# Kernel tuning notes

Measured on AMD Instinct MI355X. Metric: run time of the kernel, lower is better.

## Reference

```python
import jax, jax.numpy as jnp
import numpy as np

B, T, D, F, C = 32768, 256, 10, 512, 1  # batch, trees, max_depth, features, classes
LVL_PAD = T * 2 ** (D - 1)  # padded width of per-level node/bias tables


def setup_inputs() -> dict:
    key = jax.random.key(0)
    k = jax.random.split(key, 6)
    x = jax.random.normal(k[0], (B, F), dtype=jnp.float32)
    root_nodes = jax.random.randint(k[1], (T,), 0, F, dtype=jnp.int32)
    root_biases = jax.random.normal(k[2], (T,), dtype=jnp.float32)
    # levels 1..D-1 packed into a padded matrix; level i uses first T*2**i entries
    nodes = jax.random.randint(k[3], (D - 1, LVL_PAD), 0, F, dtype=jnp.int32)
    biases = jax.random.normal(k[4], (D - 1, LVL_PAD), dtype=jnp.float32)
    leaf_nodes = jax.random.normal(k[5], (T * 2 ** D, C), dtype=jnp.float32)
    return {"x": x, "root_nodes": root_nodes, "root_biases": root_biases,
            "nodes": nodes, "biases": biases, "leaf_nodes": leaf_nodes}


def reference(x, root_nodes, root_biases, nodes, biases, leaf_nodes):
    b = x.shape[0]
    t = root_nodes.shape[0]
    depth = nodes.shape[0] + 1
    tree_indices = 2 * jnp.arange(t, dtype=jnp.int32)  # [T]
    # root level: cond(x[:, root_nodes], root_biases) -> child index offset per tree
    prev = (x[:, root_nodes] <= root_biases).astype(jnp.int32) + tree_indices  # [B, T]
    prev = prev.reshape(-1)  # [B*T]
    for i in range(1, depth):
        width = t * (2 ** i)
        lvl_nodes = nodes[i - 1, :width]    # [T*2^i]
        lvl_biases = biases[i - 1, :width]  # [T*2^i]
        gather_idx = lvl_nodes[prev].reshape(b, t)              # [B, T] feature ids
        feats = jnp.take_along_axis(x, gather_idx, axis=1).reshape(-1)  # [B*T]
        cond = (feats <= lvl_biases[prev]).astype(jnp.int32)
        prev = 2 * prev + cond
    out = leaf_nodes[prev].reshape(b, t, -1)  # [B, T, C]
    return out
```

## Files before the change

kernel.cpp:

```cpp
#include <hip/hip_runtime.h>

constexpr int kB = 32768;
constexpr int kT = 256;
constexpr int kD = 10;
constexpr int kF = 512;
constexpr int kLvlPad = kT << (kD - 1);
constexpr int kLevels = kD - 1;

constexpr int kRows    = 32;
constexpr int kTrees   = 128;
constexpr int kChains  = 4;
constexpr int kThreads = 1024;
constexpr int kXPad    = 516;
constexpr int kOPad    = kTrees + 1;

constexpr int kP1 = kT * 2;
constexpr int kP3 = kT * 8;
constexpr int kP5 = kT * 32;
constexpr int kP7 = kT * 128;
constexpr int kFU = kT * 512;
constexpr int kO1 = 0;
constexpr int kO3 = kO1 + kP1;
constexpr int kO5 = kO3 + kP3;
constexpr int kO7 = kO5 + kP5;
constexpr int kOF = kO7 + kP7;
constexpr int kTotalRecs = kOF + kFU;
constexpr size_t kWsBytes = (size_t)kTotalRecs * 16;

__global__ __launch_bounds__(256)
void prep_kernel(const int* __restrict__ nodes, const float* __restrict__ biases,
                 const float* __restrict__ leaf_nodes, int4* __restrict__ ws)
{
    int idx = blockIdx.x * 256 + threadIdx.x;
    if (idx < kOF) {
        int i, base;
        if      (idx < kO3) { i = 1; base = kO1; }
        else if (idx < kO5) { i = 3; base = kO3; }
        else if (idx < kO7) { i = 5; base = kO5; }
        else                { i = 7; base = kO7; }
        int j = idx - base;
        const int*   nt = nodes  + (size_t)(i - 1) * kLvlPad;
        const float* bt = biases + (size_t)(i - 1) * kLvlPad;
        const int*   nc = nodes  + (size_t)i * kLvlPad;
        const float* bc = biases + (size_t)i * kLvlPad;
        unsigned int pk = (unsigned int)nt[j]
                        | ((unsigned int)nc[2 * j]     << 9)
                        | ((unsigned int)nc[2 * j + 1] << 18);
        ws[idx] = make_int4((int)pk, __float_as_int(bt[j]),
                            __float_as_int(bc[2 * j]),
                            __float_as_int(bc[2 * j + 1]));
    } else if (idx < kTotalRecs) {
        int j = idx - kOF;
        const int   n9 = nodes [(size_t)(kD - 2) * kLvlPad + j];
        const float b9 = biases[(size_t)(kD - 2) * kLvlPad + j];
        ws[idx] = make_int4(n9, __float_as_int(b9),
                            __float_as_int(leaf_nodes[2 * j]),
                            __float_as_int(leaf_nodes[2 * j + 1]));
    }
}

__global__ __launch_bounds__(kThreads)
void traverse_pair_kernel(const float* __restrict__ x,
                          const int* __restrict__ root_nodes,
                          const float* __restrict__ root_biases,
                          const int4* __restrict__ ws,
                          float* __restrict__ out)
{
    __shared__ float xs[kRows][kXPad];
    float* outs = &xs[0][0];

    const int bid = blockIdx.x;
    const int w   = bid >> 4;
    const int s   = bid & 15;
    const int bx  = w * 8 + (s & 7);
    const int by  = s >> 3;
    const int b0  = bx * kRows;
    const int t0  = by * kTrees;
    const int tid = threadIdx.x;

    {
        const float4* xg = reinterpret_cast<const float4*>(x + (size_t)b0 * kF);
#pragma unroll
        for (int k = 0; k < 4; ++k) {
            int j = tid + k * kThreads;
            int r = j >> 7;
            int c = j & 127;
            float4 v = xg[(size_t)r * (kF / 4) + c];
            *reinterpret_cast<float4*>(&xs[r][c * 4]) = v;
        }
    }
    __syncthreads();

    const int r  = tid & (kRows - 1);
    const int tt = tid >> 5;
    const float* __restrict__ xrow = xs[r];

    int p[kChains];
#pragma unroll
    for (int c = 0; c < kChains; ++c) {
        int t = t0 + tt + 32 * c;
        p[c] = 2 * t + (xrow[root_nodes[t]] <= root_biases[t] ? 1 : 0);
    }

    const int4* __restrict__ P1 = ws + kO1;
    const int4* __restrict__ P3 = ws + kO3;
    const int4* __restrict__ P5 = ws + kO5;
    const int4* __restrict__ P7 = ws + kO7;
    const int4* __restrict__ FU = ws + kOF;

#define PAIR_STEP(TBL)                                                        \
    {                                                                         \
        int4 rec[kChains];                                                    \
        _Pragma("unroll")                                                     \
        for (int c = 0; c < kChains; ++c) rec[c] = TBL[p[c]];                 \
        _Pragma("unroll")                                                     \
        for (int c = 0; c < kChains; ++c) {                                   \
            unsigned int n = (unsigned int)rec[c].x;                          \
            int c0 = xrow[n & 511u] <= __int_as_float(rec[c].y) ? 1 : 0;      \
            int nc = c0 ? (int)((n >> 18) & 511u) : (int)((n >> 9) & 511u);   \
            int bb = c0 ? rec[c].w : rec[c].z;                                \
            int c1 = xrow[nc] <= __int_as_float(bb) ? 1 : 0;                  \
            p[c] = 4 * p[c] + 2 * c0 + c1;                                    \
        }                                                                     \
    }

    PAIR_STEP(P1)
    PAIR_STEP(P3)
    PAIR_STEP(P5)
    PAIR_STEP(P7)
#undef PAIR_STEP

    float leaf[kChains];
    {
        int4 rec[kChains];
#pragma unroll
        for (int c = 0; c < kChains; ++c) rec[c] = FU[p[c]];
#pragma unroll
        for (int c = 0; c < kChains; ++c) {
            leaf[c] = __int_as_float(
                xrow[rec[c].x] <= __int_as_float(rec[c].y) ? rec[c].w
                                                           : rec[c].z);
        }
    }

    __syncthreads();
#pragma unroll
    for (int c = 0; c < kChains; ++c)
        outs[r * kOPad + tt + 32 * c] = leaf[c];
    __syncthreads();

#pragma unroll
    for (int k = 0; k < 4; ++k) {
        int j    = tid + k * kThreads;
        int orow = j >> 7;
        int ocol = j & 127;
        __builtin_nontemporal_store(outs[orow * kOPad + ocol],
                                    &out[(size_t)(b0 + orow) * kT + t0 + ocol]);
    }
}

__global__ __launch_bounds__(512)
void traverse_plain_kernel(const float* __restrict__ x,
                           const int* __restrict__ root_nodes,
                           const float* __restrict__ root_biases,
                           const int* __restrict__ nodes,
                           const float* __restrict__ biases,
                           const float* __restrict__ leaf_nodes,
                           float* __restrict__ out)
{
    __shared__ float xs[16][kXPad];
    __shared__ float outs[16][65];

    const int b0  = blockIdx.x * 16;
    const int t0  = blockIdx.y * 64;
    const int tid = threadIdx.x;

    {
        const float4* xg = reinterpret_cast<const float4*>(x + (size_t)b0 * kF);
#pragma unroll
        for (int k = 0; k < 4; ++k) {
            int j = tid + k * 512;
            int r = j >> 7;
            int c = j & 127;
            float4 v = xg[(size_t)r * (kF / 4) + c];
            *reinterpret_cast<float4*>(&xs[r][c * 4]) = v;
        }
    }
    __syncthreads();

    const int r  = tid & 15;
    const int tt = tid >> 4;
    const int tA = t0 + tt;
    const int tB = t0 + tt + 32;
    const float* __restrict__ xrow = xs[r];

    int pA = 2 * tA + (xrow[root_nodes[tA]] <= root_biases[tA] ? 1 : 0);
    int pB = 2 * tB + (xrow[root_nodes[tB]] <= root_biases[tB] ? 1 : 0);

#pragma unroll
    for (int i = 1; i < kD; ++i) {
        const int*   ln = nodes  + (size_t)(i - 1) * kLvlPad;
        const float* lb = biases + (size_t)(i - 1) * kLvlPad;
        int   nA = ln[pA], nB = ln[pB];
        float bA = lb[pA], bB = lb[pB];
        pA = 2 * pA + (xrow[nA] <= bA ? 1 : 0);
        pB = 2 * pB + (xrow[nB] <= bB ? 1 : 0);
    }

    outs[r][tt]      = leaf_nodes[pA];
    outs[r][tt + 32] = leaf_nodes[pB];
    __syncthreads();

#pragma unroll
    for (int k = 0; k < 2; ++k) {
        int j    = tid + k * 512;
        int orow = j >> 6;
        int ocol = j & 63;
        __builtin_nontemporal_store(outs[orow][ocol],
                                    &out[(size_t)(b0 + orow) * kT + t0 + ocol]);
    }
}

extern "C" void kernel_launch(void* const* d_in, const int* in_sizes, int n_in,
                              void* d_out, int out_size, void* d_ws, size_t ws_size,
                              hipStream_t stream) {
    const float* x           = (const float*)d_in[0];
    const int*   root_nodes  = (const int*)d_in[1];
    const float* root_biases = (const float*)d_in[2];
    const int*   nodes       = (const int*)d_in[3];
    const float* biases      = (const float*)d_in[4];
    const float* leaf_nodes  = (const float*)d_in[5];
    float*       out         = (float*)d_out;

    if (ws_size >= kWsBytes) {
        prep_kernel<<<(kTotalRecs + 255) / 256, 256, 0, stream>>>(
            nodes, biases, leaf_nodes, (int4*)d_ws);
        const int nblocks = (kB / kRows) * (kT / kTrees);
        traverse_pair_kernel<<<nblocks, kThreads, 0, stream>>>(
            x, root_nodes, root_biases, (const int4*)d_ws, out);
    } else {
        dim3 grid(kB / 16, kT / 64);
        traverse_plain_kernel<<<grid, 512, 0, stream>>>(
            x, root_nodes, root_biases, nodes, biases, leaf_nodes, out);
    }
}
```

Measured before the change: 59.74 us.

## Pack last three tree levels and bf16 leaves into one 64-byte record

```diff
diff --git a/kernel.cpp b/kernel.cpp
--- a/kernel.cpp
+++ b/kernel.cpp
@@ -5,7 +5,6 @@
 constexpr int kD = 10;
 constexpr int kF = 512;
 constexpr int kLvlPad = kT << (kD - 1);
-constexpr int kLevels = kD - 1;
 
 constexpr int kRows    = 32;
 constexpr int kTrees   = 128;
@@ -14,30 +13,29 @@
 constexpr int kXPad    = 516;
 constexpr int kOPad    = kTrees + 1;
 
-constexpr int kP1 = kT * 2;
-constexpr int kP3 = kT * 8;
-constexpr int kP5 = kT * 32;
-constexpr int kP7 = kT * 128;
-constexpr int kFU = kT * 512;
 constexpr int kO1 = 0;
-constexpr int kO3 = kO1 + kP1;
-constexpr int kO5 = kO3 + kP3;
-constexpr int kO7 = kO5 + kP5;
-constexpr int kOF = kO7 + kP7;
-constexpr int kTotalRecs = kOF + kFU;
-constexpr size_t kWsBytes = (size_t)kTotalRecs * 16;
+constexpr int kO3 = 512;
+constexpr int kO5 = 2560;
+constexpr int kOT = 10752;
+constexpr int kNT = 32768;
+constexpr int kPrepThreads = kOT + kNT;
+constexpr size_t kWsBytes = (size_t)(kOT + 4 * kNT) * 16;
+
+__device__ __forceinline__ unsigned bf16_rne(float f) {
+    unsigned u = __float_as_uint(f);
+    return (u + 0x7fffu + ((u >> 16) & 1u)) >> 16;
+}
 
 __global__ __launch_bounds__(256)
 void prep_kernel(const int* __restrict__ nodes, const float* __restrict__ biases,
                  const float* __restrict__ leaf_nodes, int4* __restrict__ ws)
 {
     int idx = blockIdx.x * 256 + threadIdx.x;
-    if (idx < kOF) {
+    if (idx < kOT) {
         int i, base;
         if      (idx < kO3) { i = 1; base = kO1; }
         else if (idx < kO5) { i = 3; base = kO3; }
-        else if (idx < kO7) { i = 5; base = kO5; }
-        else                { i = 7; base = kO7; }
+        else                { i = 5; base = kO5; }
         int j = idx - base;
         const int*   nt = nodes  + (size_t)(i - 1) * kLvlPad;
         const float* bt = biases + (size_t)(i - 1) * kLvlPad;
@@ -49,13 +47,37 @@
         ws[idx] = make_int4((int)pk, __float_as_int(bt[j]),
                             __float_as_int(bc[2 * j]),
                             __float_as_int(bc[2 * j + 1]));
-    } else if (idx < kTotalRecs) {
-        int j = idx - kOF;
-        const int   n9 = nodes [(size_t)(kD - 2) * kLvlPad + j];
-        const float b9 = biases[(size_t)(kD - 2) * kLvlPad + j];
-        ws[idx] = make_int4(n9, __float_as_int(b9),
-                            __float_as_int(leaf_nodes[2 * j]),
-                            __float_as_int(leaf_nodes[2 * j + 1]));
+    } else if (idx < kPrepThreads) {
+        int j = idx - kOT;
+        const int*   n7 = nodes  + (size_t)6 * kLvlPad;
+        const float* b7 = biases + (size_t)6 * kLvlPad;
+        const int*   n8 = nodes  + (size_t)7 * kLvlPad;
+        const float* b8 = biases + (size_t)7 * kLvlPad;
+        const int*   n9 = nodes  + (size_t)8 * kLvlPad;
+        const float* b9 = biases + (size_t)8 * kLvlPad;
+        unsigned a7  = (unsigned)n7[j];
+        unsigned a8L = (unsigned)n8[2 * j],     a8R = (unsigned)n8[2 * j + 1];
+        unsigned a9LL = (unsigned)n9[4 * j],     a9LR = (unsigned)n9[4 * j + 1];
+        unsigned a9RL = (unsigned)n9[4 * j + 2], a9RR = (unsigned)n9[4 * j + 3];
+        int4 q0 = make_int4((int)(a7  | (a8L  << 16)),
+                            (int)(a8R | (a9LL << 16)),
+                            (int)(a9LR | (a9RL << 16)),
+                            (int)a9RR);
+        int4 q1 = make_int4(__float_as_int(b7[j]),
+                            __float_as_int(b8[2 * j]),
+                            __float_as_int(b8[2 * j + 1]),
+                            __float_as_int(b9[4 * j]));
+        unsigned l0 = bf16_rne(leaf_nodes[8 * j])     | (bf16_rne(leaf_nodes[8 * j + 1]) << 16);
+        unsigned l1 = bf16_rne(leaf_nodes[8 * j + 2]) | (bf16_rne(leaf_nodes[8 * j + 3]) << 16);
+        unsigned l2 = bf16_rne(leaf_nodes[8 * j + 4]) | (bf16_rne(leaf_nodes[8 * j + 5]) << 16);
+        unsigned l3 = bf16_rne(leaf_nodes[8 * j + 6]) | (bf16_rne(leaf_nodes[8 * j + 7]) << 16);
+        int4 q2 = make_int4(__float_as_int(b9[4 * j + 1]),
+                            __float_as_int(b9[4 * j + 2]),
+                            __float_as_int(b9[4 * j + 3]),
+                            (int)l0);
+        int4 q3 = make_int4((int)l1, (int)l2, (int)l3, 0);
+        int4* rp = ws + kOT + 4 * j;
+        rp[0] = q0; rp[1] = q1; rp[2] = q2; rp[3] = q3;
     }
 }
 
@@ -105,8 +127,7 @@
     const int4* __restrict__ P1 = ws + kO1;
     const int4* __restrict__ P3 = ws + kO3;
     const int4* __restrict__ P5 = ws + kO5;
-    const int4* __restrict__ P7 = ws + kO7;
-    const int4* __restrict__ FU = ws + kOF;
+    const int4* __restrict__ T9 = ws + kOT;
 
 #define PAIR_STEP(TBL)                                                        \
     {                                                                         \
@@ -127,19 +148,33 @@
     PAIR_STEP(P1)
     PAIR_STEP(P3)
     PAIR_STEP(P5)
-    PAIR_STEP(P7)
 #undef PAIR_STEP
 
     float leaf[kChains];
     {
-        int4 rec[kChains];
-#pragma unroll
-        for (int c = 0; c < kChains; ++c) rec[c] = FU[p[c]];
+        int4 q0[kChains], q1[kChains], q2[kChains], q3[kChains];
 #pragma unroll
         for (int c = 0; c < kChains; ++c) {
-            leaf[c] = __int_as_float(
-                xrow[rec[c].x] <= __int_as_float(rec[c].y) ? rec[c].w
-                                                           : rec[c].z);
+            const int4* rp = T9 + 4 * p[c];
+            q0[c] = rp[0]; q1[c] = rp[1]; q2[c] = rp[2]; q3[c] = rp[3];
+        }
+#pragma unroll
+        for (int c = 0; c < kChains; ++c) {
+            unsigned w0 = (unsigned)q0[c].x, w1 = (unsigned)q0[c].y;
+            unsigned w2 = (unsigned)q0[c].z, w3 = (unsigned)q0[c].w;
+            int c7 = xrow[w0 & 0xffffu] <= __int_as_float(q1[c].x) ? 1 : 0;
+            unsigned n8 = c7 ? (w1 & 0xffffu) : (w0 >> 16);
+            float    b8 = __int_as_float(c7 ? q1[c].z : q1[c].y);
+            int c8 = xrow[n8] <= b8 ? 1 : 0;
+            unsigned n9 = c7 ? (c8 ? (w3 & 0xffffu) : (w2 >> 16))
+                             : (c8 ? (w2 & 0xffffu) : (w1 >> 16));
+            float    b9 = __int_as_float(c7 ? (c8 ? q2[c].z : q2[c].y)
+                                            : (c8 ? q2[c].x : q1[c].w));
+            int c9 = xrow[n9] <= b9 ? 1 : 0;
+            unsigned lp = (unsigned)(c7 ? (c8 ? q3[c].z : q3[c].y)
+                                        : (c8 ? q3[c].x : q2[c].w));
+            unsigned lb = c9 ? (lp >> 16) : (lp & 0xffffu);
+            leaf[c] = __int_as_float((int)(lb << 16));
         }
     }
 
@@ -233,7 +268,7 @@
     float*       out         = (float*)d_out;
 
     if (ws_size >= kWsBytes) {
-        prep_kernel<<<(kTotalRecs + 255) / 256, 256, 0, stream>>>(
+        prep_kernel<<<(kPrepThreads + 255) / 256, 256, 0, stream>>>(
             nodes, biases, leaf_nodes, (int4*)d_ws);
         const int nblocks = (kB / kRows) * (kT / kTrees);
         traverse_pair_kernel<<<nblocks, kThreads, 0, stream>>>(
```

Result: slower. 83.32 us (+39.5%).
